# Kernel tuning notes

Hardware: AMD Instinct MI355X
Metric: run time of the kernel (lower is better)

The kernel has to match this reference:

```python
import jax, jax.numpy as jnp
import numpy as np

EPS = 1e-12

def l2_normalize(x):
    # matches torch.nn.functional.normalize(p=2): x / max(||x||, eps)
    n = jnp.sqrt(jnp.sum(x * x, axis=-1, keepdims=True))
    return x / jnp.maximum(n, EPS)

def setup_inputs() -> dict:
    key = jax.random.key(0)
    k1, k2, k3, k4 = jax.random.split(key, 4)
    batch, n_neg, E, n_rel = 512, 2048, 256, 1000
    return {
        "head_emb": jax.random.normal(k1, (batch, E), dtype=jnp.float32),
        "tail_emb": jax.random.normal(k2, (1, n_neg, E), dtype=jnp.float32),
        "relation_embedding": jax.random.normal(k3, (n_rel, 2 * E), dtype=jnp.float32),
        "relation_id": jax.random.randint(k4, (batch,), 0, n_rel, dtype=jnp.int64),
    }

def reference(head_emb, tail_emb, relation_embedding, relation_id):
    # PairRE.score_tails with negative_sample_sharing=True, scoring_norm=2,
    # normalize_entities=True.
    E = head_emb.shape[-1]
    rel = relation_embedding[relation_id]          # (batch, 2E)
    r_h, r_t = rel[:, :E], rel[:, E:]              # (batch, E) each
    h = l2_normalize(head_emb)                     # (batch, E)
    t = l2_normalize(tail_emb)                     # (1, n_neg, E)
    t = t.reshape(1, -1, E)                        # negative sample sharing
    # diff: (batch, n_neg, E)
    diff = t * r_t[:, None, :] - (h * r_h)[:, None, :]
    # p=2 norm reduction over embedding dim -> (batch, n_neg)
    return -jnp.sqrt(jnp.sum(diff * diff, axis=-1))
```

## Files before the change

### kernel.cpp

```cpp
#include <hip/hip_runtime.h>
#include <hip/hip_bf16.h>


#define B_DIM 512
#define N_DIM 2048
#define E_DIM 256
#define K_DIM 512
#define NSTEP 16
#define FRAG_US 512

typedef __attribute__((ext_vector_type(8))) __bf16 bf16x8;
typedef __attribute__((ext_vector_type(4))) float f32x4;

__device__ inline ushort f2bf(float x) {
    __hip_bfloat16 h = __float2bfloat16(x);
    union { __hip_bfloat16 b; ushort u; } cv; cv.b = h; return cv.u;
}

__device__ inline float block_reduce_sum_256(float v, float* buf) {
#pragma unroll
    for (int o = 32; o > 0; o >>= 1) v += __shfl_down(v, o, 64);
    const int lane = threadIdx.x & 63, wid = threadIdx.x >> 6;
    __syncthreads();
    if (lane == 0) buf[wid] = v;
    __syncthreads();
    return buf[0] + buf[1] + buf[2] + buf[3];
}

__global__ __launch_bounds__(256) void prep_kernel(
        const float* __restrict__ head, const float* __restrict__ tail,
        const float* __restrict__ rel,  const int* __restrict__ rid,
        ushort* __restrict__ Tbig, ushort* __restrict__ Abig,
        float* __restrict__ cvec) {
    __shared__ float buf[4];
    const int tid = threadIdx.x;
    const int blk = blockIdx.x;
    if (blk < N_DIM) {
        const int n = blk;
        const float tv = tail[(size_t)n * E_DIM + tid];
        const float tot = block_reduce_sum_256(tv * tv, buf);
        const float inv = 1.0f / fmaxf(sqrtf(tot), 1e-12f);
        if (tid < 64) {
            const int c = tid, k0 = c * 8;
            const bool sqr = (k0 < E_DIM);
            const int e0 = sqr ? k0 : k0 - E_DIM;
            const float4 f0 = *(const float4*)(tail + (size_t)n * E_DIM + e0);
            const float4 f1 = *(const float4*)(tail + (size_t)n * E_DIM + e0 + 4);
            const float v[8] = {f0.x, f0.y, f0.z, f0.w, f1.x, f1.y, f1.z, f1.w};
            ushort u[8];
#pragma unroll
            for (int j = 0; j < 8; ++j) {
                float x = v[j] * inv;
                if (sqr) x *= x;
                u[j] = f2bf(x);
            }
            const int s = k0 >> 5, q = (k0 >> 3) & 3, g = n >> 4, m = n & 15;
            *(uint4*)(Tbig + (size_t)((g * 16 + s) * 64 + q * 16 + m) * 8) = *(const uint4*)u;
        }
    } else {
        const int b = blk - N_DIM;
        const int id = rid[b];
        const float hv = head[(size_t)b * E_DIM + tid];
        const float rh = rel[(size_t)id * (2 * E_DIM) + tid];
        const float s1 = block_reduce_sum_256(hv * hv, buf);
        const float inv = 1.0f / fmaxf(sqrtf(s1), 1e-12f);
        const float Hh = hv * inv * rh;
        const float s2 = block_reduce_sum_256(Hh * Hh, buf);
        if (tid == 0) cvec[b] = s2;
        if (tid < 64) {
            const int c = tid, k0 = c * 8;
            const bool sqr = (k0 < E_DIM);
            const int e0 = sqr ? k0 : k0 - E_DIM;
            const float4 rt0 = *(const float4*)(rel + (size_t)id * (2 * E_DIM) + E_DIM + e0);
            const float4 rt1 = *(const float4*)(rel + (size_t)id * (2 * E_DIM) + E_DIM + e0 + 4);
            const float rt[8] = {rt0.x, rt0.y, rt0.z, rt0.w, rt1.x, rt1.y, rt1.z, rt1.w};
            float v[8];
            if (sqr) {
#pragma unroll
                for (int j = 0; j < 8; ++j) v[j] = rt[j] * rt[j];
            } else {
                const float4 h0 = *(const float4*)(head + (size_t)b * E_DIM + e0);
                const float4 h1 = *(const float4*)(head + (size_t)b * E_DIM + e0 + 4);
                const float4 rh0 = *(const float4*)(rel + (size_t)id * (2 * E_DIM) + e0);
                const float4 rh1 = *(const float4*)(rel + (size_t)id * (2 * E_DIM) + e0 + 4);
                const float hh[8] = {h0.x, h0.y, h0.z, h0.w, h1.x, h1.y, h1.z, h1.w};
                const float rr[8] = {rh0.x, rh0.y, rh0.z, rh0.w, rh1.x, rh1.y, rh1.z, rh1.w};
#pragma unroll
                for (int j = 0; j < 8; ++j) v[j] = -2.0f * rt[j] * (hh[j] * inv * rr[j]);
            }
            ushort u[8];
#pragma unroll
            for (int j = 0; j < 8; ++j) u[j] = f2bf(v[j]);
            const int s = k0 >> 5, q = (k0 >> 3) & 3, g = b >> 4, m = b & 15;
            *(uint4*)(Abig + (size_t)((g * 16 + s) * 64 + q * 16 + m) * 8) = *(const uint4*)u;
        }
    }
}

__global__ __launch_bounds__(256) void score_kernel(
        const ushort* __restrict__ Tbig, const ushort* __restrict__ Abig,
        const float* __restrict__ cvec, float* __restrict__ out) {
    const int tid = threadIdx.x, lane = tid & 63, wv = tid >> 6;
    const int w = blockIdx.x * 4 + wv;
    const int p_b = w >> 6;
    const int p_n = w & 63;
    const int b0 = p_b * 16, n0 = p_n * 32;

    const ushort* Ab  = Abig + (size_t)(p_b * NSTEP) * FRAG_US + lane * 8;
    const ushort* Tb0 = Tbig + (size_t)(p_n * 2 * NSTEP) * FRAG_US + lane * 8;
    const ushort* Tb1 = Tb0 + (size_t)NSTEP * FRAG_US;

    f32x4 acc0 = {0.f, 0.f, 0.f, 0.f}, acc1 = {0.f, 0.f, 0.f, 0.f};

    bf16x8 a_c  = *(const bf16x8*)(Ab);
    bf16x8 b0_c = *(const bf16x8*)(Tb0);
    bf16x8 b1_c = *(const bf16x8*)(Tb1);
#pragma unroll
    for (int s = 0; s < NSTEP - 1; ++s) {
        const bf16x8 a_n  = *(const bf16x8*)(Ab  + (s + 1) * FRAG_US);
        const bf16x8 b0_n = *(const bf16x8*)(Tb0 + (s + 1) * FRAG_US);
        const bf16x8 b1_n = *(const bf16x8*)(Tb1 + (s + 1) * FRAG_US);
        acc0 = __builtin_amdgcn_mfma_f32_16x16x32_bf16(a_c, b0_c, acc0, 0, 0, 0);
        acc1 = __builtin_amdgcn_mfma_f32_16x16x32_bf16(a_c, b1_c, acc1, 0, 0, 0);
        a_c = a_n; b0_c = b0_n; b1_c = b1_n;
    }
    acc0 = __builtin_amdgcn_mfma_f32_16x16x32_bf16(a_c, b0_c, acc0, 0, 0, 0);
    acc1 = __builtin_amdgcn_mfma_f32_16x16x32_bf16(a_c, b1_c, acc1, 0, 0, 0);

    const int ml = lane & 15, q = lane >> 4;
#pragma unroll
    for (int r = 0; r < 4; ++r) {
        const int b = b0 + q * 4 + r;
        const float cb = cvec[b];
        out[(size_t)b * N_DIM + n0 + ml]      = -sqrtf(fmaxf(acc0[r] + cb, 0.f));
        out[(size_t)b * N_DIM + n0 + 16 + ml] = -sqrtf(fmaxf(acc1[r] + cb, 0.f));
    }
}

__global__ __launch_bounds__(256) void fallback_kernel(
        const float* __restrict__ head, const float* __restrict__ tail,
        const float* __restrict__ rel,  const int* __restrict__ rid,
        float* __restrict__ out) {
    __shared__ float Hh[E_DIM];
    __shared__ float RT[E_DIM];
    __shared__ float buf[4];
    const int b = blockIdx.x;
    const int tid = threadIdx.x;
    const float hv = head[(size_t)b * E_DIM + tid];
    const int id = rid[b];
    const float rh = rel[(size_t)id * (2 * E_DIM) + tid];
    const float rt = rel[(size_t)id * (2 * E_DIM) + E_DIM + tid];
    const float tot = block_reduce_sum_256(hv * hv, buf);
    const float inv = 1.0f / fmaxf(sqrtf(tot), 1e-12f);
    const float HhV = hv * inv * rh;
    Hh[tid] = HhV; RT[tid] = rt;
    const float c = block_reduce_sum_256(HhV * HhV, buf);
    __syncthreads();
    for (int n = tid; n < N_DIM; n += 256) {
        float S1 = 0.f, S2 = 0.f, Stt = 0.f;
        for (int e = 0; e < E_DIM; ++e) {
            const float tv = tail[(size_t)n * E_DIM + e];
            const float p = tv * RT[e];
            S1 += p * p; S2 += p * Hh[e]; Stt += tv * tv;
        }
        const float al = 1.0f / fmaxf(sqrtf(Stt), 1e-12f);
        const float x = al * al * S1 - 2.0f * al * S2 + c;
        out[(size_t)b * N_DIM + n] = -sqrtf(fmaxf(x, 0.f));
    }
}

extern "C" void kernel_launch(void* const* d_in, const int* in_sizes, int n_in,
                              void* d_out, int out_size, void* d_ws, size_t ws_size,
                              hipStream_t stream) {
    const float* head = (const float*)d_in[0];
    const float* tail = (const float*)d_in[1];
    const float* rel  = (const float*)d_in[2];
    const int*   rid  = (const int*)d_in[3];
    float* out = (float*)d_out;

    const size_t needT = (size_t)N_DIM * K_DIM * sizeof(ushort);
    const size_t needA = (size_t)B_DIM * K_DIM * sizeof(ushort);
    const size_t needC = (size_t)B_DIM * sizeof(float);
    if (ws_size >= needT + needA + needC) {
        ushort* Tbig = (ushort*)d_ws;
        ushort* Abig = Tbig + (size_t)N_DIM * K_DIM;
        float*  cvec = (float*)(Abig + (size_t)B_DIM * K_DIM);
        prep_kernel<<<N_DIM + B_DIM, 256, 0, stream>>>(head, tail, rel, rid,
                                                       Tbig, Abig, cvec);
        score_kernel<<<B_DIM * N_DIM / (4 * 16 * 32), 256, 0, stream>>>(
            Tbig, Abig, cvec, out);
    } else {
        fallback_kernel<<<B_DIM, 256, 0, stream>>>(head, tail, rel, rid, out);
    }
}
```

Measured before the change: 70.35 us.

## Use one wave per row in prep and 2x2 wave tiling in score kernel

```diff
diff --git a/kernel.cpp b/kernel.cpp
--- a/kernel.cpp
+++ b/kernel.cpp
@@ -17,14 +17,10 @@
     union { __hip_bfloat16 b; ushort u; } cv; cv.b = h; return cv.u;
 }
 
-__device__ inline float block_reduce_sum_256(float v, float* buf) {
-#pragma unroll
-    for (int o = 32; o > 0; o >>= 1) v += __shfl_down(v, o, 64);
-    const int lane = threadIdx.x & 63, wid = threadIdx.x >> 6;
-    __syncthreads();
-    if (lane == 0) buf[wid] = v;
-    __syncthreads();
-    return buf[0] + buf[1] + buf[2] + buf[3];
+__device__ inline float wave_sum(float v) {
+#pragma unroll
+    for (int m = 1; m < 64; m <<= 1) v += __shfl_xor(v, m, 64);
+    return v;
 }
 
 __global__ __launch_bounds__(256) void prep_kernel(
@@ -32,68 +28,68 @@
         const float* __restrict__ rel,  const int* __restrict__ rid,
         ushort* __restrict__ Tbig, ushort* __restrict__ Abig,
         float* __restrict__ cvec) {
-    __shared__ float buf[4];
-    const int tid = threadIdx.x;
-    const int blk = blockIdx.x;
-    if (blk < N_DIM) {
-        const int n = blk;
-        const float tv = tail[(size_t)n * E_DIM + tid];
-        const float tot = block_reduce_sum_256(tv * tv, buf);
-        const float inv = 1.0f / fmaxf(sqrtf(tot), 1e-12f);
-        if (tid < 64) {
-            const int c = tid, k0 = c * 8;
-            const bool sqr = (k0 < E_DIM);
-            const int e0 = sqr ? k0 : k0 - E_DIM;
-            const float4 f0 = *(const float4*)(tail + (size_t)n * E_DIM + e0);
-            const float4 f1 = *(const float4*)(tail + (size_t)n * E_DIM + e0 + 4);
-            const float v[8] = {f0.x, f0.y, f0.z, f0.w, f1.x, f1.y, f1.z, f1.w};
-            ushort u[8];
-#pragma unroll
-            for (int j = 0; j < 8; ++j) {
-                float x = v[j] * inv;
-                if (sqr) x *= x;
-                u[j] = f2bf(x);
-            }
-            const int s = k0 >> 5, q = (k0 >> 3) & 3, g = n >> 4, m = n & 15;
-            *(uint4*)(Tbig + (size_t)((g * 16 + s) * 64 + q * 16 + m) * 8) = *(const uint4*)u;
+    const int tid = threadIdx.x, lane = tid & 63, wv = tid >> 6;
+    const int w = blockIdx.x * 4 + wv;
+    const int s_ = lane >> 2, q = lane & 3;
+    const int k0 = lane * 8;
+    const bool sqr = (k0 < E_DIM);
+    const int e0 = k0 & (E_DIM - 1);
+
+    if (w < N_DIM) {
+        const int n = w;
+        const float* row = tail + (size_t)n * E_DIM;
+        const float4 v4 = ((const float4*)row)[lane];
+        const float s = wave_sum(v4.x * v4.x + v4.y * v4.y + v4.z * v4.z + v4.w * v4.w);
+        const float inv = 1.0f / fmaxf(sqrtf(s), 1e-12f);
+        const float4 f0 = *(const float4*)(row + e0);
+        const float4 f1 = *(const float4*)(row + e0 + 4);
+        const float v[8] = {f0.x, f0.y, f0.z, f0.w, f1.x, f1.y, f1.z, f1.w};
+        ushort u[8];
+#pragma unroll
+        for (int j = 0; j < 8; ++j) {
+            float x = v[j] * inv;
+            if (sqr) x *= x;
+            u[j] = f2bf(x);
         }
+        const int g = n >> 4, m = n & 15;
+        *(uint4*)(Tbig + (size_t)((g * 16 + s_) * 64 + q * 16 + m) * 8) = *(const uint4*)u;
     } else {
-        const int b = blk - N_DIM;
+        const int b = w - N_DIM;
         const int id = rid[b];
-        const float hv = head[(size_t)b * E_DIM + tid];
-        const float rh = rel[(size_t)id * (2 * E_DIM) + tid];
-        const float s1 = block_reduce_sum_256(hv * hv, buf);
+        const float* hrow  = head + (size_t)b * E_DIM;
+        const float* rhrow = rel + (size_t)id * (2 * E_DIM);
+        const float* rtrow = rhrow + E_DIM;
+        const float4 h4  = ((const float4*)hrow)[lane];
+        const float4 rh4 = ((const float4*)rhrow)[lane];
+        const float s1 = wave_sum(h4.x * h4.x + h4.y * h4.y + h4.z * h4.z + h4.w * h4.w);
         const float inv = 1.0f / fmaxf(sqrtf(s1), 1e-12f);
-        const float Hh = hv * inv * rh;
-        const float s2 = block_reduce_sum_256(Hh * Hh, buf);
-        if (tid == 0) cvec[b] = s2;
-        if (tid < 64) {
-            const int c = tid, k0 = c * 8;
-            const bool sqr = (k0 < E_DIM);
-            const int e0 = sqr ? k0 : k0 - E_DIM;
-            const float4 rt0 = *(const float4*)(rel + (size_t)id * (2 * E_DIM) + E_DIM + e0);
-            const float4 rt1 = *(const float4*)(rel + (size_t)id * (2 * E_DIM) + E_DIM + e0 + 4);
-            const float rt[8] = {rt0.x, rt0.y, rt0.z, rt0.w, rt1.x, rt1.y, rt1.z, rt1.w};
-            float v[8];
-            if (sqr) {
-#pragma unroll
-                for (int j = 0; j < 8; ++j) v[j] = rt[j] * rt[j];
-            } else {
-                const float4 h0 = *(const float4*)(head + (size_t)b * E_DIM + e0);
-                const float4 h1 = *(const float4*)(head + (size_t)b * E_DIM + e0 + 4);
-                const float4 rh0 = *(const float4*)(rel + (size_t)id * (2 * E_DIM) + e0);
-                const float4 rh1 = *(const float4*)(rel + (size_t)id * (2 * E_DIM) + e0 + 4);
-                const float hh[8] = {h0.x, h0.y, h0.z, h0.w, h1.x, h1.y, h1.z, h1.w};
-                const float rr[8] = {rh0.x, rh0.y, rh0.z, rh0.w, rh1.x, rh1.y, rh1.z, rh1.w};
-#pragma unroll
-                for (int j = 0; j < 8; ++j) v[j] = -2.0f * rt[j] * (hh[j] * inv * rr[j]);
-            }
-            ushort u[8];
-#pragma unroll
-            for (int j = 0; j < 8; ++j) u[j] = f2bf(v[j]);
-            const int s = k0 >> 5, q = (k0 >> 3) & 3, g = b >> 4, m = b & 15;
-            *(uint4*)(Abig + (size_t)((g * 16 + s) * 64 + q * 16 + m) * 8) = *(const uint4*)u;
+        const float p0 = h4.x * inv * rh4.x, p1 = h4.y * inv * rh4.y;
+        const float p2 = h4.z * inv * rh4.z, p3 = h4.w * inv * rh4.w;
+        const float s2 = wave_sum(p0 * p0 + p1 * p1 + p2 * p2 + p3 * p3);
+        if (lane == 0) cvec[b] = s2;
+
+        const float4 rt0 = *(const float4*)(rtrow + e0);
+        const float4 rt1 = *(const float4*)(rtrow + e0 + 4);
+        const float rt[8] = {rt0.x, rt0.y, rt0.z, rt0.w, rt1.x, rt1.y, rt1.z, rt1.w};
+        float v[8];
+        if (sqr) {
+#pragma unroll
+            for (int j = 0; j < 8; ++j) v[j] = rt[j] * rt[j];
+        } else {
+            const float4 h0 = *(const float4*)(hrow + e0);
+            const float4 h1 = *(const float4*)(hrow + e0 + 4);
+            const float4 r0 = *(const float4*)(rhrow + e0);
+            const float4 r1 = *(const float4*)(rhrow + e0 + 4);
+            const float hh[8] = {h0.x, h0.y, h0.z, h0.w, h1.x, h1.y, h1.z, h1.w};
+            const float rr[8] = {r0.x, r0.y, r0.z, r0.w, r1.x, r1.y, r1.z, r1.w};
+#pragma unroll
+            for (int j = 0; j < 8; ++j) v[j] = -2.0f * rt[j] * (hh[j] * inv * rr[j]);
         }
+        ushort u[8];
+#pragma unroll
+        for (int j = 0; j < 8; ++j) u[j] = f2bf(v[j]);
+        const int g = b >> 4, m = b & 15;
+        *(uint4*)(Abig + (size_t)((g * 16 + s_) * 64 + q * 16 + m) * 8) = *(const uint4*)u;
     }
 }
 
@@ -101,13 +97,12 @@
         const ushort* __restrict__ Tbig, const ushort* __restrict__ Abig,
         const float* __restrict__ cvec, float* __restrict__ out) {
     const int tid = threadIdx.x, lane = tid & 63, wv = tid >> 6;
-    const int w = blockIdx.x * 4 + wv;
-    const int p_b = w >> 6;
-    const int p_n = w & 63;
-    const int b0 = p_b * 16, n0 = p_n * 32;
-
-    const ushort* Ab  = Abig + (size_t)(p_b * NSTEP) * FRAG_US + lane * 8;
-    const ushort* Tb0 = Tbig + (size_t)(p_n * 2 * NSTEP) * FRAG_US + lane * 8;
+    const int p_n = blockIdx.x, b_super = blockIdx.y;
+    const int gA  = b_super * 2 + (wv & 1);
+    const int gT0 = p_n * 4 + (wv >> 1) * 2;
+
+    const ushort* Ab  = Abig + (size_t)gA * NSTEP * FRAG_US + lane * 8;
+    const ushort* Tb0 = Tbig + (size_t)gT0 * NSTEP * FRAG_US + lane * 8;
     const ushort* Tb1 = Tb0 + (size_t)NSTEP * FRAG_US;
 
     f32x4 acc0 = {0.f, 0.f, 0.f, 0.f}, acc1 = {0.f, 0.f, 0.f, 0.f};
@@ -128,6 +123,8 @@
     acc1 = __builtin_amdgcn_mfma_f32_16x16x32_bf16(a_c, b1_c, acc1, 0, 0, 0);
 
     const int ml = lane & 15, q = lane >> 4;
+    const int b0 = gA * 16;
+    const int n0 = gT0 * 16;
 #pragma unroll
     for (int r = 0; r < 4; ++r) {
         const int b = b0 + q * 4 + r;
@@ -135,6 +132,16 @@
         out[(size_t)b * N_DIM + n0 + ml]      = -sqrtf(fmaxf(acc0[r] + cb, 0.f));
         out[(size_t)b * N_DIM + n0 + 16 + ml] = -sqrtf(fmaxf(acc1[r] + cb, 0.f));
     }
+}
+
+__device__ inline float block_reduce_sum_256(float v, float* buf) {
+#pragma unroll
+    for (int o = 32; o > 0; o >>= 1) v += __shfl_down(v, o, 64);
+    const int lane = threadIdx.x & 63, wid = threadIdx.x >> 6;
+    __syncthreads();
+    if (lane == 0) buf[wid] = v;
+    __syncthreads();
+    return buf[0] + buf[1] + buf[2] + buf[3];
 }
 
 __global__ __launch_bounds__(256) void fallback_kernel(
@@ -185,10 +192,10 @@
         ushort* Tbig = (ushort*)d_ws;
         ushort* Abig = Tbig + (size_t)N_DIM * K_DIM;
         float*  cvec = (float*)(Abig + (size_t)B_DIM * K_DIM);
-        prep_kernel<<<N_DIM + B_DIM, 256, 0, stream>>>(head, tail, rel, rid,
-                                                       Tbig, Abig, cvec);
-        score_kernel<<<B_DIM * N_DIM / (4 * 16 * 32), 256, 0, stream>>>(
-            Tbig, Abig, cvec, out);
+        prep_kernel<<<(N_DIM + B_DIM) / 4, 256, 0, stream>>>(head, tail, rel, rid,
+                                                             Tbig, Abig, cvec);
+        dim3 grid(N_DIM / 64, B_DIM / 32);
+        score_kernel<<<grid, 256, 0, stream>>>(Tbig, Abig, cvec, out);
     } else {
         fallback_kernel<<<B_DIM, 256, 0, stream>>>(head, tail, rel, rid, out);
     }
```

New measurement: 68.46 us. 1.03x faster.
